# Kernel tuning notes

Hardware: AMD Instinct MI355X
Metric: run time of the kernel (lower is better)

Reference implementation:

```python
import jax, jax.numpy as jnp
import numpy as np

N_BRANCH, N_LAYER = 4, 3
B, T, D_IN = 4, 1024, 32
D_MODEL, D_INNER, D_STATE, D_CONV, DT_RANK = 128, 256, 16, 4, 8
EMBED = 64
MAX_NORM = 10.0  # safe_expmap0 tangent-norm clip
EPS = 1e-7


def setup_inputs() -> dict:
    key = jax.random.key(0)
    ks = jax.random.split(key, 12)
    def nrm(k, shp, s=0.02):
        return s * jax.random.normal(k, shp, dtype=jnp.float32)
    A_init = jnp.log(jnp.arange(1, D_STATE + 1, dtype=jnp.float32))
    return {
        "trend": jax.random.normal(ks[0], (B, T, D_IN), jnp.float32),
        "seasonal_coarse": jax.random.normal(ks[1], (B, T, D_IN), jnp.float32),
        "seasonal_fine": jax.random.normal(ks[2], (B, T, D_IN), jnp.float32),
        "residual": jax.random.normal(ks[3], (B, T, D_IN), jnp.float32),
        "W_ip": nrm(ks[4], (N_BRANCH, D_IN, D_MODEL)),
        "b_ip": jnp.zeros((N_BRANCH, D_MODEL), jnp.float32),
        "W_in": nrm(ks[5], (N_BRANCH, N_LAYER, D_MODEL, 2 * D_INNER)),
        "conv_w": nrm(ks[6], (N_BRANCH, N_LAYER, D_INNER, D_CONV), 0.1),
        "conv_b": jnp.zeros((N_BRANCH, N_LAYER, D_INNER), jnp.float32),
        "W_x": nrm(ks[7], (N_BRANCH, N_LAYER, D_INNER, DT_RANK + 2 * D_STATE)),
        "W_dt": nrm(ks[8], (N_BRANCH, N_LAYER, DT_RANK, D_INNER), 0.1),
        "b_dt": jnp.full((N_BRANCH, N_LAYER, D_INNER), -4.6, jnp.float32),  # softplus ~ 0.01
        "A_log": jnp.broadcast_to(A_init, (N_BRANCH, N_LAYER, D_INNER, D_STATE)),
        "D_param": jnp.ones((N_BRANCH, N_LAYER, D_INNER), jnp.float32),
        "W_out": nrm(ks[9], (N_BRANCH, N_LAYER, D_INNER, D_MODEL)),
        "W_op": nrm(ks[10], (N_BRANCH, D_MODEL, EMBED)),
        "b_op": jnp.zeros((N_BRANCH, EMBED), jnp.float32),
        "eff_scale": jnp.asarray(0.1, jnp.float32),
    }


def _mamba_layer(x, Win, cw, cb, Wx, Wdt, bdt, Alog, Dp, Wout):
    # x: [B, T, d_model]
    Tlen = x.shape[1]
    xz = x @ Win                                   # [B,T,2*di]
    xp, z = jnp.split(xz, 2, axis=-1)
    # causal depthwise conv1d, kernel D_CONV
    xpad = jnp.pad(xp, ((0, 0), (D_CONV - 1, 0), (0, 0)))
    xc = sum(xpad[:, k:k + Tlen, :] * cw[:, k] for k in range(D_CONV))
    xc = jax.nn.silu(xc + cb)                      # [B,T,di]
    dbl = xc @ Wx                                  # [B,T,r+2s]
    dt = jax.nn.softplus(dbl[..., :DT_RANK] @ Wdt + bdt)   # [B,T,di]
    Bm = dbl[..., DT_RANK:DT_RANK + D_STATE]       # [B,T,s]
    Cm = dbl[..., DT_RANK + D_STATE:]              # [B,T,s]
    A = -jnp.exp(Alog)                             # [di,s]
    dA = jnp.exp(dt[..., None] * A)                # [B,T,di,s]
    dBx = (dt * xc)[..., None] * Bm[:, :, None, :] # [B,T,di,s]

    def step(h, inp):
        dA_t, dBx_t, C_t = inp
        h = dA_t * h + dBx_t
        return h, jnp.einsum('bds,bs->bd', h, C_t)

    h0 = jnp.zeros((x.shape[0], D_INNER, D_STATE), x.dtype)
    _, ys = jax.lax.scan(step, h0, (jnp.swapaxes(dA, 0, 1),
                                     jnp.swapaxes(dBx, 0, 1),
                                     jnp.swapaxes(Cm, 0, 1)))
    y = jnp.swapaxes(ys, 0, 1) + Dp * xc
    return (y * jax.nn.silu(z)) @ Wout


def _embed(x, Wip, bip, Wins, cws, cbs, Wxs, Wdts, bdts, Alogs, Dps, Wouts, Wop, bop):
    h = x @ Wip + bip
    for l in range(N_LAYER):
        h = _mamba_layer(h, Wins[l], cws[l], cbs[l], Wxs[l], Wdts[l], bdts[l],
                         Alogs[l], Dps[l], Wouts[l])
    return h.mean(axis=1) @ Wop + bop              # [B, EMBED]


def _expmap0(v):
    # safe expmap0 on Lorentz (k=1): clip tangent norm at MAX_NORM
    n = jnp.linalg.norm(v, axis=-1, keepdims=True)
    nc = jnp.clip(n, EPS, MAX_NORM)
    v = v * (nc / jnp.maximum(n, EPS))
    return jnp.concatenate([jnp.cosh(nc), jnp.sinh(nc) / nc * v], axis=-1)


def _projx(x):
    sp = x[..., 1:]
    t = jnp.sqrt(1.0 + jnp.sum(sp * sp, axis=-1, keepdims=True))
    return jnp.concatenate([t, sp], axis=-1)


def _logmap0(x):
    sp = x[..., 1:]
    t = jnp.maximum(x[..., :1], 1.0 + EPS)
    d = jnp.arccosh(t)
    spn = jnp.maximum(jnp.linalg.norm(sp, axis=-1, keepdims=True), EPS)
    return d * sp / spn


def _forward(trend, seasonal_coarse, seasonal_fine, residual,
             W_ip, b_ip, W_in, conv_w, conv_b, W_x, W_dt, b_dt,
             A_log, D_param, W_out, W_op, b_op, eff_scale):
    xs = [trend, seasonal_coarse, seasonal_fine, residual]
    z_t = [
        _embed(xs[b], W_ip[b], b_ip[b], W_in[b], conv_w[b], conv_b[b], W_x[b],
               W_dt[b], b_dt[b], A_log[b], D_param[b], W_out[b], W_op[b], b_op[b])
        for b in range(N_BRANCH)
    ]
    es = jnp.tanh(eff_scale)
    z_h = [_projx(_expmap0(z * es)) for z in z_t]
    us = [_logmap0(zh) for zh in z_h]
    combined_tangent = us[0] + us[1] + us[2] + us[3]
    combined_h = _projx(_expmap0(combined_tangent * es))
    return (*z_t, *z_h, combined_tangent, combined_h)


def reference(trend, seasonal_coarse, seasonal_fine, residual,
              W_ip, b_ip, W_in, conv_w, conv_b, W_x, W_dt, b_dt,
              A_log, D_param, W_out, W_op, b_op, eff_scale):
    return _forward(trend, seasonal_coarse, seasonal_fine, residual,
                    W_ip, b_ip, W_in, conv_w, conv_b, W_x, W_dt, b_dt,
                    A_log, D_param, W_out, W_op, b_op, eff_scale)
```

## Files before the change

kernel.cpp:

```cpp
#include <hip/hip_runtime.h>
#include <math.h>

#define NBR 4
#define NLAY 3
#define Bk 4
#define Tk 1024
#define DIN 32
#define DMODEL 128
#define DINNER 256
#define DSTATE 16
#define DTRANK 8
#define EMBEDk 64
#define BT (Bk*Tk)
#define EPSF 1e-7f
#define MAXNF 10.0f
#define LCH 64
#define NCH (Tk/LCH)
#define UF 8
#define NWB 320

typedef __bf16 bf16x8 __attribute__((ext_vector_type(8)));
typedef float  f32x4  __attribute__((ext_vector_type(4)));
typedef unsigned short u16x8 __attribute__((ext_vector_type(8)));

__device__ __forceinline__ float siluf(float x){ return x / (1.f + __expf(-x)); }
__device__ __forceinline__ float softplusf(float x){ return (x > 20.f) ? x : log1pf(__expf(x)); }
__device__ __forceinline__ unsigned short f2b(float x){
    union { float f; unsigned u; } v; v.f = x;
    unsigned r = v.u + 0x7FFF + ((v.u >> 16) & 1);
    return (unsigned short)(r >> 16);
}
__device__ __forceinline__ float b2f(unsigned short u){
    union { unsigned u; float f; } v; v.u = ((unsigned)u) << 16; return v.f;
}

__device__ __forceinline__ void dA_pow(float q, float* dA){
    dA[0] = q;             dA[1] = q * q;
    dA[2] = dA[1] * dA[0]; dA[3] = dA[1] * dA[1];
    dA[4] = dA[3] * dA[0]; dA[5] = dA[3] * dA[1];
    dA[6] = dA[3] * dA[2]; dA[7] = dA[3] * dA[3];
    #pragma unroll
    for (int s = 8; s < 16; ++s) dA[s] = dA[s - 8] * dA[7];
}
__device__ __forceinline__ void dA_exp(float dtv, const float* Aa, float* dA){
    #pragma unroll
    for (int s = 0; s < 16; ++s) dA[s] = __expf(dtv * Aa[s]);
}

template<int MODE>
__global__ __launch_bounds__(256) void bgemm_k(
    const unsigned short* __restrict__ Ab, long aBr, int K,
    const unsigned short* __restrict__ Bt, long bBr,
    float* __restrict__ C0, long c0Br,
    float* __restrict__ C1, long c1Br,
    unsigned short* __restrict__ Cb, long cbBr,
    const float* __restrict__ bias, long biasBr)
{
    const int br = blockIdx.z;
    Ab += (long)br * aBr;
    Bt += (long)br * bBr;
    if (MODE == 1 || MODE == 3) C0 += (long)br * c0Br;
    if (MODE == 0 || MODE == 3) C1 += (long)br * c1Br;
    if (MODE == 0) Cb += (long)br * cbBr;
    if (MODE == 3) bias += (long)br * biasBr;
    const int m0 = blockIdx.x * 64, n0 = blockIdx.y * 64;
    __shared__ __align__(16) unsigned short As[8 * 64 * 8];
    __shared__ __align__(16) unsigned short Bs[8 * 64 * 8];
    const int tid = threadIdx.x;
    const int lane = tid & 63, w = tid >> 6;
    const int wm = w >> 1, wn = w & 1;
    const int quad = lane >> 4, l15 = lane & 15;
    f32x4 acc00 = {0,0,0,0}, acc01 = {0,0,0,0}, acc10 = {0,0,0,0}, acc11 = {0,0,0,0};
    for (int kc = 0; kc < K; kc += 64) {
        #pragma unroll
        for (int it = 0; it < 2; ++it) {
            const int c = tid + it * 256;
            const int r = c & 63, kch = c >> 6;
            *(u16x8*)&As[(kch * 64 + r) * 8] =
                *(const u16x8*)(Ab + (long)(m0 + r) * K + kc + kch * 8);
            *(u16x8*)&Bs[(kch * 64 + r) * 8] =
                *(const u16x8*)(Bt + (long)(n0 + r) * K + kc + kch * 8);
        }
        __syncthreads();
        #pragma unroll
        for (int k0 = 0; k0 < 64; k0 += 32) {
            const int kch = (k0 >> 3) + quad;
            bf16x8 a0 = *(const bf16x8*)&As[(kch * 64 + wm * 32 +      l15) * 8];
            bf16x8 a1 = *(const bf16x8*)&As[(kch * 64 + wm * 32 + 16 + l15) * 8];
            bf16x8 b0 = *(const bf16x8*)&Bs[(kch * 64 + wn * 32 +      l15) * 8];
            bf16x8 b1 = *(const bf16x8*)&Bs[(kch * 64 + wn * 32 + 16 + l15) * 8];
            acc00 = __builtin_amdgcn_mfma_f32_16x16x32_bf16(a0, b0, acc00, 0, 0, 0);
            acc01 = __builtin_amdgcn_mfma_f32_16x16x32_bf16(a0, b1, acc01, 0, 0, 0);
            acc10 = __builtin_amdgcn_mfma_f32_16x16x32_bf16(a1, b0, acc10, 0, 0, 0);
            acc11 = __builtin_amdgcn_mfma_f32_16x16x32_bf16(a1, b1, acc11, 0, 0, 0);
        }
        __syncthreads();
    }
    #pragma unroll
    for (int e = 0; e < 4; ++e) {
        f32x4 a = (e == 0) ? acc00 : (e == 1) ? acc01 : (e == 2) ? acc10 : acc11;
        const int msub = (e >> 1) * 16, nsub = (e & 1) * 16;
        const int col = n0 + wn * 32 + nsub + l15;
        #pragma unroll
        for (int r = 0; r < 4; ++r) {
            const int row = m0 + wm * 32 + msub + quad * 4 + r;
            const float v = a[r];
            if (MODE == 0) {
                if (n0 < 256) Cb[(long)row * 256 + col] = f2b(v);
                else          C1[(long)row * 256 + (col - 256)] = siluf(v);
            } else if (MODE == 1) {
                C0[(long)row * 128 + col] = v;
            } else {
                if (col < 256)      C0[(long)row * 256 + col] = softplusf(v + bias[col]);
                else if (col < 288) C1[(long)row * 32 + (col - 256)] = v;
            }
        }
    }
}

__global__ __launch_bounds__(256) void prepT_k(
    const float* __restrict__ W, unsigned short* __restrict__ o,
    int Kd, int Nd, long wBr, long oBr)
{
    const int br = blockIdx.z;
    W += (long)br * wBr; o += (long)br * oBr;
    const int n0 = blockIdx.x * 64, k0 = blockIdx.y * 64;
    __shared__ float tile[64][65];
    const int t = threadIdx.x;
    #pragma unroll
    for (int i = 0; i < 16; ++i) {
        int idx = t + i * 256;
        int kl = idx >> 6, nl = idx & 63;
        tile[kl][nl] = W[(long)(k0 + kl) * Nd + n0 + nl];
    }
    __syncthreads();
    #pragma unroll
    for (int i = 0; i < 16; ++i) {
        int idx = t + i * 256;
        int nl = idx >> 6, kl = idx & 63;
        o[(long)(n0 + nl) * Kd + k0 + kl] = f2b(tile[kl][nl]);
    }
}

__global__ __launch_bounds__(256) void sgemmW_k(
    const float* __restrict__ Wout, const float* __restrict__ Win,
    float* __restrict__ Wtmp)
{
    const int z = blockIdx.z, p = z >> 2, br = z & 3;
    const float* A  = Wout + (long)(br * NLAY + p) * DINNER * DMODEL;
    const float* Bw = Win  + (long)(br * NLAY + p + 1) * DMODEL * 512;
    float* C = Wtmp + (long)z * DINNER * 512;
    const int m0 = blockIdx.x * 64, n0 = blockIdx.y * 64;
    __shared__ float As[32][68];
    __shared__ float Bs[32][68];
    const int tid = threadIdx.x;
    const int tx = tid & 15, ty = tid >> 4;
    float acc[4][4] = {};
    for (int kc = 0; kc < DMODEL; kc += 32) {
        #pragma unroll
        for (int it = 0; it < 2; ++it) {
            int id = tid + it * 256;
            int r = id >> 3, c4 = (id & 7) << 2;
            float4 v = *(const float4*)(A + (long)(m0 + r) * DMODEL + kc + c4);
            As[c4+0][r] = v.x; As[c4+1][r] = v.y; As[c4+2][r] = v.z; As[c4+3][r] = v.w;
            int rb = id >> 4, cb = (id & 15) << 2;
            *(float4*)&Bs[rb][cb] = *(const float4*)(Bw + (long)(kc + rb) * 512 + n0 + cb);
        }
        __syncthreads();
        #pragma unroll
        for (int kk = 0; kk < 32; ++kk) {
            float4 a4 = *(const float4*)&As[kk][ty << 2];
            float4 b4 = *(const float4*)&Bs[kk][tx << 2];
            float av[4] = {a4.x, a4.y, a4.z, a4.w};
            float bv[4] = {b4.x, b4.y, b4.z, b4.w};
            #pragma unroll
            for (int i = 0; i < 4; ++i)
                #pragma unroll
                for (int j = 0; j < 4; ++j)
                    acc[i][j] = fmaf(av[i], bv[j], acc[i][j]);
        }
        __syncthreads();
    }
    #pragma unroll
    for (int i = 0; i < 4; ++i) {
        int row = m0 + (ty << 2) + i, col = n0 + (tx << 2);
        float4 v4; v4.x = acc[i][0]; v4.y = acc[i][1]; v4.z = acc[i][2]; v4.w = acc[i][3];
        *(float4*)(C + (long)row * 512 + col) = v4;
    }
}

__global__ __launch_bounds__(256) void prepC_k(
    const float* __restrict__ Wx, const float* __restrict__ Wdt,
    unsigned short* __restrict__ o)
{
    const int n = blockIdx.x, bl = blockIdx.y;
    const int k = threadIdx.x;
    const float* WxP = Wx + (long)bl * DINNER * 40;
    float v;
    if (n < 256) {
        const float* WdtP = Wdt + (long)bl * DTRANK * DINNER;
        float s = 0.f;
        #pragma unroll
        for (int r = 0; r < 8; ++r) s = fmaf(WxP[k * 40 + r], WdtP[r * DINNER + n], s);
        v = s;
    } else if (n < 288) {
        v = WxP[k * 40 + 8 + (n - 256)];
    } else {
        v = 0.f;
    }
    o[(long)bl * NWB * DINNER + (long)n * DINNER + k] = f2b(v);
}

__global__ __launch_bounds__(256) void proj_k(
    const float* __restrict__ A0, const float* __restrict__ A1,
    const float* __restrict__ A2, const float* __restrict__ A3,
    const float* __restrict__ Bw, const float* __restrict__ bias,
    unsigned short* __restrict__ Cb)
{
    const int br = blockIdx.z;
    const float* A = (br == 1) ? A1 : (br == 2) ? A2 : (br == 3) ? A3 : A0;
    Bw   += (long)br * DIN * DMODEL;
    bias += (long)br * DMODEL;
    Cb   += (long)br * BT * DMODEL;
    const int m0 = blockIdx.x * 64, n0 = blockIdx.y * 64;
    __shared__ float As[32][68];
    __shared__ float Bs[32][68];
    const int tid = threadIdx.x;
    const int tx = tid & 15, ty = tid >> 4;
    float acc[4][4] = {};
    {
        #pragma unroll
        for (int it = 0; it < 2; ++it) {
            int id = tid + it * 256;
            int r = id >> 3, c4 = (id & 7) << 2;
            float4 v = *(const float4*)(A + (long)(m0 + r) * DIN + c4);
            As[c4+0][r] = v.x; As[c4+1][r] = v.y; As[c4+2][r] = v.z; As[c4+3][r] = v.w;
            int rb = id >> 4, cb = (id & 15) << 2;
            *(float4*)&Bs[rb][cb] = *(const float4*)(Bw + (long)rb * DMODEL + n0 + cb);
        }
        __syncthreads();
        #pragma unroll
        for (int kk = 0; kk < 32; ++kk) {
            float4 a4 = *(const float4*)&As[kk][ty << 2];
            float4 b4 = *(const float4*)&Bs[kk][tx << 2];
            float av[4] = {a4.x, a4.y, a4.z, a4.w};
            float bv[4] = {b4.x, b4.y, b4.z, b4.w};
            #pragma unroll
            for (int i = 0; i < 4; ++i)
                #pragma unroll
                for (int j = 0; j < 4; ++j)
                    acc[i][j] = fmaf(av[i], bv[j], acc[i][j]);
        }
    }
    const int col = n0 + (tx << 2);
    float bs[4];
    #pragma unroll
    for (int j = 0; j < 4; ++j) bs[j] = bias[col + j];
    #pragma unroll
    for (int i = 0; i < 4; ++i) {
        const int row = m0 + (ty << 2) + i;
        #pragma unroll
        for (int j = 0; j < 4; ++j)
            Cb[(long)row * DMODEL + col + j] = f2b(acc[i][j] + bs[j]);
    }
}

__global__ __launch_bounds__(256) void conv_k(
    const unsigned short* __restrict__ xp, const float* __restrict__ cw,
    const float* __restrict__ cb, unsigned short* __restrict__ xcb, int layer)
{
    const int br = blockIdx.y;
    const long base = (long)br * BT * DINNER;
    const int idx = blockIdx.x * 256 + threadIdx.x;
    const int d = idx & (DINNER - 1);
    const int row = idx >> 8;
    const int t = row & (Tk - 1);
    const float4 w4 = *(const float4*)(cw + ((long)(br * NLAY + layer) * DINNER + d) * 4);
    const float wv[4] = {w4.x, w4.y, w4.z, w4.w};
    float acc = cb[(br * NLAY + layer) * DINNER + d];
    const unsigned short* xpb = xp + base + idx;
    #pragma unroll
    for (int k = 0; k < 4; ++k) {
        int tt = t + k - 3;
        if (tt >= 0) acc = fmaf(b2f(xpb[(long)(k - 3) * DINNER]), wv[k], acc);
    }
    xcb[base + idx] = f2b(siluf(acc));
}

__global__ __launch_bounds__(256) void scan1_k(
    const float* __restrict__ dtb, const unsigned short* __restrict__ xcb,
    const float* __restrict__ bcb, const float* __restrict__ Alog,
    float* __restrict__ recbuf, int layer)
{
    const int c = blockIdx.x, b = blockIdx.y, br = blockIdx.z;
    const int d = threadIdx.x;
    const float* Ap = Alog + ((long)(br * NLAY + layer) * DINNER + d) * DSTATE;
    float Aa[16];
    bool pw = true;
    #pragma unroll
    for (int s = 0; s < 16; ++s) {
        Aa[s] = -__expf(Ap[s]);
        pw = pw && (fabsf(Aa[s] + (float)(s + 1)) < 1e-3f);
    }
    const long rbase = (long)br * BT + (long)b * Tk + (long)c * LCH;
    const float* dtp = dtb + rbase * DINNER + d;
    const unsigned short* xcp = xcb + rbase * DINNER + d;
    __shared__ float bcs[LCH * 32];
    {
        const float4* g = (const float4*)(bcb + rbase * 32);
        float4* l = (float4*)bcs;
        l[d] = g[d]; l[d + 256] = g[d + 256];
    }
    float dtc[UF], xcc[UF];
    #pragma unroll
    for (int u = 0; u < UF; ++u) {
        dtc[u] = dtp[(long)u * DINNER];
        xcc[u] = b2f(xcp[(long)u * DINNER]);
    }
    __syncthreads();
    float h[16];
    #pragma unroll
    for (int s = 0; s < 16; ++s) h[s] = 0.f;
    float sumdt = 0.f;
    for (int base = 0; base < LCH; base += UF) {
        const int nb = (base + UF < LCH) ? base + UF : base;
        float dtn[UF], xcn[UF];
        #pragma unroll
        for (int u = 0; u < UF; ++u) {
            dtn[u] = dtp[(long)(nb + u) * DINNER];
            xcn[u] = b2f(xcp[(long)(nb + u) * DINNER]);
        }
        #pragma unroll
        for (int u = 0; u < UF; ++u) {
            const int t = base + u;
            const float dtv = dtc[u];
            const float dtxc = dtv * xcc[u];
            sumdt += dtv;
            float dA[16];
            if (pw) dA_pow(__expf(-dtv), dA);
            else    dA_exp(dtv, Aa, dA);
            const float* bcT = bcs + t * 32;
            #pragma unroll
            for (int s = 0; s < 16; ++s)
                h[s] = fmaf(dA[s], h[s], dtxc * bcT[s]);
        }
        #pragma unroll
        for (int u = 0; u < UF; ++u) { dtc[u] = dtn[u]; xcc[u] = xcn[u]; }
    }
    float* sb = recbuf + (((long)(br * 4 + b) * (NCH - 1) + c) * 17) * 256 + d;
    #pragma unroll
    for (int s = 0; s < 16; ++s) sb[s * 256] = h[s];
    sb[16 * 256] = sumdt;
}

__global__ __launch_bounds__(256) void scan3_k(
    const float* __restrict__ dtb, const unsigned short* __restrict__ xcb,
    const float* __restrict__ bcb, const float* __restrict__ zb,
    const float* __restrict__ Alog, const float* __restrict__ Dpar,
    const float* __restrict__ recbuf, unsigned short* __restrict__ yzb, int layer)
{
    const int c = blockIdx.x, b = blockIdx.y, br = blockIdx.z;
    const int d = threadIdx.x;
    const float* Ap = Alog + ((long)(br * NLAY + layer) * DINNER + d) * DSTATE;
    float Aa[16];
    bool pw = true;
    #pragma unroll
    for (int s = 0; s < 16; ++s) {
        Aa[s] = -__expf(Ap[s]);
        pw = pw && (fabsf(Aa[s] + (float)(s + 1)) < 1e-3f);
    }
    float h[16];
    #pragma unroll
    for (int s = 0; s < 16; ++s) h[s] = 0.f;
    if (c > 0) {
        const float* recB = recbuf + ((long)(br * 4 + b) * (NCH - 1)) * 17 * 256 + d;
        float rh[16], rs;
        #pragma unroll
        for (int s = 0; s < 16; ++s) rh[s] = recB[s * 256];
        rs = recB[16 * 256];
        for (int cc = 0; cc < c; ++cc) {
            float nh[16], ns = 0.f;
            if (cc + 1 < c) {
                const float* r2 = recB + (long)(cc + 1) * 17 * 256;
                #pragma unroll
                for (int s = 0; s < 16; ++s) nh[s] = r2[s * 256];
                ns = r2[16 * 256];
            } else {
                #pragma unroll
                for (int s = 0; s < 16; ++s) nh[s] = 0.f;
            }
            float P[16];
            if (pw) dA_pow(__expf(-rs), P);
            else    dA_exp(rs, Aa, P);
            #pragma unroll
            for (int s = 0; s < 16; ++s) h[s] = fmaf(h[s], P[s], rh[s]);
            #pragma unroll
            for (int s = 0; s < 16; ++s) rh[s] = nh[s];
            rs = ns;
        }
    }
    const float Dp = Dpar[(br * NLAY + layer) * DINNER + d];
    const long rbase = (long)br * BT + (long)b * Tk + (long)c * LCH;
    const float* dtp = dtb + rbase * DINNER + d;
    const unsigned short* xcp = xcb + rbase * DINNER + d;
    const float* zp  = zb  + rbase * DINNER + d;
    unsigned short* yp = yzb + rbase * DINNER + d;
    __shared__ float bcs[LCH * 32];
    {
        const float4* g = (const float4*)(bcb + rbase * 32);
        float4* l = (float4*)bcs;
        l[d] = g[d]; l[d + 256] = g[d + 256];
    }
    float dtc[UF], xcc[UF], zc[UF];
    #pragma unroll
    for (int u = 0; u < UF; ++u) {
        dtc[u] = dtp[(long)u * DINNER];
        xcc[u] = b2f(xcp[(long)u * DINNER]);
        zc[u]  = zp[(long)u * DINNER];
    }
    __syncthreads();
    for (int base = 0; base < LCH; base += UF) {
        const int nb = (base + UF < LCH) ? base + UF : base;
        float dtn[UF], xcn[UF], zn[UF];
        #pragma unroll
        for (int u = 0; u < UF; ++u) {
            dtn[u] = dtp[(long)(nb + u) * DINNER];
            xcn[u] = b2f(xcp[(long)(nb + u) * DINNER]);
            zn[u]  = zp[(long)(nb + u) * DINNER];
        }
        #pragma unroll
        for (int u = 0; u < UF; ++u) {
            const int t = base + u;
            const float dtv = dtc[u], xcv = xcc[u];
            const float dtxc = dtv * xcv;
            float dA[16];
            if (pw) dA_pow(__expf(-dtv), dA);
            else    dA_exp(dtv, Aa, dA);
            const float* bcT = bcs + t * 32;
            #pragma unroll
            for (int s = 0; s < 16; ++s)
                h[s] = fmaf(dA[s], h[s], dtxc * bcT[s]);
            float y0 = 0.f, y1 = 0.f, y2 = 0.f, y3 = 0.f;
            #pragma unroll
            for (int s = 0; s < 16; s += 4) {
                y0 = fmaf(h[s+0], bcT[16+s+0], y0);
                y1 = fmaf(h[s+1], bcT[16+s+1], y1);
                y2 = fmaf(h[s+2], bcT[16+s+2], y2);
                y3 = fmaf(h[s+3], bcT[16+s+3], y3);
            }
            const float y = (y0 + y1) + (y2 + y3) + Dp * xcv;
            yp[(long)t * DINNER] = f2b(y * zc[u]);
        }
        #pragma unroll
        for (int u = 0; u < UF; ++u) { dtc[u] = dtn[u]; xcc[u] = xcn[u]; zc[u] = zn[u]; }
    }
}

__global__ __launch_bounds__(128) void meanop_k(
    const float* __restrict__ hbuf, const float* __restrict__ Wop,
    const float* __restrict__ bop, float* __restrict__ outzt)
{
    const int br = blockIdx.x >> 2, b = blockIdx.x & 3;
    const int tid = threadIdx.x;
    const float* hp = hbuf + ((long)br * BT + (long)b * Tk) * DMODEL + tid;
    float s = 0.f;
    for (int t = 0; t < Tk; ++t) s += hp[(long)t * DMODEL];
    __shared__ float hm[DMODEL];
    hm[tid] = s * (1.0f / Tk);
    __syncthreads();
    if (tid < EMBEDk) {
        float acc = bop[br * EMBEDk + tid];
        for (int k = 0; k < DMODEL; ++k)
            acc = fmaf(hm[k], Wop[(long)br * DMODEL * EMBEDk + k * EMBEDk + tid], acc);
        outzt[br * (Bk * EMBEDk) + b * EMBEDk + tid] = acc;
    }
}

__global__ __launch_bounds__(64) void final_k(
    const float* __restrict__ zt, float* __restrict__ out, const float* __restrict__ eff)
{
    const float es = tanhf(eff[0]);
    __shared__ float us[NBR][Bk][EMBEDk];
    const int t = threadIdx.x;
    if (t < 16) {
        const int br = t >> 2, b = t & 3;
        const float* z = zt + br * (Bk * EMBEDk) + b * EMBEDk;
        float n2 = 0.f;
        for (int e = 0; e < EMBEDk; ++e) { float v = z[e] * es; n2 = fmaf(v, v, n2); }
        const float n  = sqrtf(n2);
        const float nc = fminf(fmaxf(n, EPSF), MAXNF);
        const float sc = nc / fmaxf(n, EPSF);
        const float sh = sinhf(nc) / nc;
        const float fac = es * sc * sh;
        float* zh = out + 1024 + br * (Bk * (EMBEDk + 1)) + b * (EMBEDk + 1);
        float sp2 = 0.f;
        for (int e = 0; e < EMBEDk; ++e) {
            float spv = z[e] * fac;
            sp2 = fmaf(spv, spv, sp2);
            zh[1 + e] = spv;
            us[br][b][e] = spv;
        }
        const float t0 = sqrtf(1.f + sp2);
        zh[0] = t0;
        const float dd  = acoshf(fmaxf(t0, 1.f + EPSF));
        const float spn = fmaxf(sqrtf(sp2), EPSF);
        const float rr  = dd / spn;
        for (int e = 0; e < EMBEDk; ++e) us[br][b][e] *= rr;
    }
    __syncthreads();
    if (t < 4) {
        const int b = t;
        float ct[EMBEDk];
        float* cto = out + 2064 + b * EMBEDk;
        for (int e = 0; e < EMBEDk; ++e) {
            float v = us[0][b][e] + us[1][b][e] + us[2][b][e] + us[3][b][e];
            ct[e] = v; cto[e] = v;
        }
        float n2 = 0.f;
        for (int e = 0; e < EMBEDk; ++e) { float v = ct[e] * es; n2 = fmaf(v, v, n2); }
        const float n  = sqrtf(n2);
        const float nc = fminf(fmaxf(n, EPSF), MAXNF);
        const float sc = nc / fmaxf(n, EPSF);
        const float sh = sinhf(nc) / nc;
        const float fac = es * sc * sh;
        float* ch = out + 2320 + b * (EMBEDk + 1);
        float sp2 = 0.f;
        for (int e = 0; e < EMBEDk; ++e) {
            float spv = ct[e] * fac;
            sp2 = fmaf(spv, spv, sp2);
            ch[1 + e] = spv;
        }
        ch[0] = sqrtf(1.f + sp2);
    }
}

extern "C" void kernel_launch(void* const* d_in, const int* in_sizes, int n_in,
                              void* d_out, int out_size, void* d_ws, size_t ws_size,
                              hipStream_t stream)
{
    const float* X0 = (const float*)d_in[0];
    const float* X1 = (const float*)d_in[1];
    const float* X2 = (const float*)d_in[2];
    const float* X3 = (const float*)d_in[3];
    const float* W_ip   = (const float*)d_in[4];
    const float* b_ip   = (const float*)d_in[5];
    const float* W_in   = (const float*)d_in[6];
    const float* conv_w = (const float*)d_in[7];
    const float* conv_b = (const float*)d_in[8];
    const float* W_x    = (const float*)d_in[9];
    const float* W_dt   = (const float*)d_in[10];
    const float* b_dt   = (const float*)d_in[11];
    const float* A_log  = (const float*)d_in[12];
    const float* D_par  = (const float*)d_in[13];
    const float* W_out  = (const float*)d_in[14];
    const float* W_op   = (const float*)d_in[15];
    const float* b_op   = (const float*)d_in[16];
    const float* eff    = (const float*)d_in[17];
    float* out = (float*)d_out;
    float* ws  = (float*)d_ws;

    float* buf_z  = ws;
    float* buf_dt = buf_z  + (long)NBR * BT * DINNER;
    float* buf_bc = buf_dt + (long)NBR * BT * DINNER;
    float* buf_h  = buf_bc + (long)NBR * BT * 32;
    float* recbuf = buf_h  + (long)NBR * BT * DMODEL;
    float* Wtmp   = recbuf + (long)16 * (NCH - 1) * 17 * 256;
    unsigned short* h_bf  = (unsigned short*)(Wtmp + (long)8 * DINNER * 512);
    unsigned short* xp_bf = h_bf  + (long)NBR * BT * DMODEL;
    unsigned short* xc_bf = xp_bf + (long)NBR * BT * DINNER;
    unsigned short* yz_bf = xc_bf + (long)NBR * BT * DINNER;
    unsigned short* Win0T = yz_bf + (long)NBR * BT * DINNER;
    unsigned short* WfT   = Win0T + (long)NBR * 512 * DMODEL;
    unsigned short* WcT   = WfT   + (long)8 * 512 * DINNER;
    unsigned short* Wo2T  = WcT   + (long)NBR * NLAY * NWB * DINNER;

    prepT_k<<<dim3(8, 2, NBR), 256, 0, stream>>>(
        W_in, Win0T, DMODEL, 512, (long)NLAY * DMODEL * 512, (long)512 * DMODEL);
    sgemmW_k<<<dim3(4, 8, 8), 256, 0, stream>>>(W_out, W_in, Wtmp);
    prepT_k<<<dim3(8, 4, 8), 256, 0, stream>>>(
        Wtmp, WfT, DINNER, 512, (long)DINNER * 512, (long)512 * DINNER);
    prepC_k<<<dim3(NWB, NBR * NLAY), 256, 0, stream>>>(W_x, W_dt, WcT);
    prepT_k<<<dim3(2, 4, NBR), 256, 0, stream>>>(
        W_out + (long)2 * DINNER * DMODEL, Wo2T, DINNER, DMODEL,
        (long)NLAY * DINNER * DMODEL, (long)DMODEL * DINNER);

    proj_k<<<dim3(BT / 64, DMODEL / 64, NBR), 256, 0, stream>>>(
        X0, X1, X2, X3, W_ip, b_ip, h_bf);

    for (int l = 0; l < NLAY; ++l) {
        if (l == 0) {
            bgemm_k<0><<<dim3(BT / 64, 8, NBR), 256, 0, stream>>>(
                h_bf, (long)BT * DMODEL, DMODEL,
                Win0T, (long)512 * DMODEL,
                nullptr, 0, buf_z, (long)BT * DINNER,
                xp_bf, (long)BT * DINNER, nullptr, 0);
        } else {
            bgemm_k<0><<<dim3(BT / 64, 8, NBR), 256, 0, stream>>>(
                yz_bf, (long)BT * DINNER, DINNER,
                WfT + (long)(l - 1) * 4 * 512 * DINNER, (long)512 * DINNER,
                nullptr, 0, buf_z, (long)BT * DINNER,
                xp_bf, (long)BT * DINNER, nullptr, 0);
        }
        conv_k<<<dim3((BT * DINNER) / 256, NBR), 256, 0, stream>>>(
            xp_bf, conv_w, conv_b, xc_bf, l);
        bgemm_k<3><<<dim3(BT / 64, NWB / 64, NBR), 256, 0, stream>>>(
            xc_bf, (long)BT * DINNER, DINNER,
            WcT + (long)l * NWB * DINNER, (long)NLAY * NWB * DINNER,
            buf_dt, (long)BT * DINNER, buf_bc, (long)BT * 32,
            nullptr, 0, b_dt + l * DINNER, (long)NLAY * DINNER);
        scan1_k<<<dim3(NCH - 1, Bk, NBR), 256, 0, stream>>>(
            buf_dt, xc_bf, buf_bc, A_log, recbuf, l);
        scan3_k<<<dim3(NCH, Bk, NBR), 256, 0, stream>>>(
            buf_dt, xc_bf, buf_bc, buf_z, A_log, D_par, recbuf, yz_bf, l);
        if (l == NLAY - 1) {
            bgemm_k<1><<<dim3(BT / 64, DMODEL / 64, NBR), 256, 0, stream>>>(
                yz_bf, (long)BT * DINNER, DINNER,
                Wo2T, (long)DMODEL * DINNER,
                buf_h, (long)BT * DMODEL, nullptr, 0,
                nullptr, 0, nullptr, 0);
        }
    }

    meanop_k<<<16, 128, 0, stream>>>(buf_h, W_op, b_op, out);
    final_k<<<1, 64, 0, stream>>>(out, out, eff);
}
```

Baseline: 471.8 us.

## Fuse prep kernels, store z as bf16, and reduce the final GEMM into a mean via atomics

Merges the weight transpose, combined-weight prep and input projection kernels into one launch. The z gate is now stored as bf16 instead of fp32, halving its write and read traffic. The last output GEMM no longer writes the full hidden tensor; it reduces its tile into per-batch column sums with atomicAdd, and the output projection moves into final_k, removing meanop_k. This cuts launches and memory traffic, but float atomics make the summation order nondeterministic, the zero-init of the accumulator sits inside the sgemmW kernel, and bf16 z adds rounding error.

```diff
diff --git a/kernel.cpp b/kernel.cpp
--- a/kernel.cpp
+++ b/kernel.cpp
@@ -54,15 +54,17 @@
     float* __restrict__ C0, long c0Br,
     float* __restrict__ C1, long c1Br,
     unsigned short* __restrict__ Cb, long cbBr,
+    unsigned short* __restrict__ Cb2, long cb2Br,
+    float* __restrict__ Mb,
     const float* __restrict__ bias, long biasBr)
 {
     const int br = blockIdx.z;
     Ab += (long)br * aBr;
     Bt += (long)br * bBr;
-    if (MODE == 1 || MODE == 3) C0 += (long)br * c0Br;
-    if (MODE == 0 || MODE == 3) C1 += (long)br * c1Br;
-    if (MODE == 0) Cb += (long)br * cbBr;
-    if (MODE == 3) bias += (long)br * biasBr;
+    if (MODE == 3) { C0 += (long)br * c0Br; C1 += (long)br * c1Br;
+                     bias += (long)br * biasBr; }
+    if (MODE == 0) { Cb += (long)br * cbBr; Cb2 += (long)br * cb2Br; }
+    if (MODE == 1) { Mb += (long)br * (Bk * DMODEL); }
     const int m0 = blockIdx.x * 64, n0 = blockIdx.y * 64;
     __shared__ __align__(16) unsigned short As[8 * 64 * 8];
     __shared__ __align__(16) unsigned short Bs[8 * 64 * 8];
@@ -96,6 +98,16 @@
         }
         __syncthreads();
     }
+    if (MODE == 1) {
+        float s0 = 0.f, s1 = 0.f;
+        #pragma unroll
+        for (int r = 0; r < 4; ++r) { s0 += acc00[r] + acc10[r];
+                                      s1 += acc01[r] + acc11[r]; }
+        const int bidx = m0 >> 10;
+        atomicAdd(&Mb[bidx * DMODEL + n0 + wn * 32 + l15], s0);
+        atomicAdd(&Mb[bidx * DMODEL + n0 + wn * 32 + 16 + l15], s1);
+        return;
+    }
     #pragma unroll
     for (int e = 0; e < 4; ++e) {
         f32x4 a = (e == 0) ? acc00 : (e == 1) ? acc01 : (e == 2) ? acc10 : acc11;
@@ -107,9 +119,7 @@
             const float v = a[r];
             if (MODE == 0) {
                 if (n0 < 256) Cb[(long)row * 256 + col] = f2b(v);
-                else          C1[(long)row * 256 + (col - 256)] = siluf(v);
-            } else if (MODE == 1) {
-                C0[(long)row * 128 + col] = v;
+                else          Cb2[(long)row * 256 + (col - 256)] = f2b(siluf(v));
             } else {
                 if (col < 256)      C0[(long)row * 256 + col] = softplusf(v + bias[col]);
                 else if (col < 288) C1[(long)row * 32 + (col - 256)] = v;
@@ -118,34 +128,13 @@
     }
 }
 
-__global__ __launch_bounds__(256) void prepT_k(
-    const float* __restrict__ W, unsigned short* __restrict__ o,
-    int Kd, int Nd, long wBr, long oBr)
-{
-    const int br = blockIdx.z;
-    W += (long)br * wBr; o += (long)br * oBr;
-    const int n0 = blockIdx.x * 64, k0 = blockIdx.y * 64;
-    __shared__ float tile[64][65];
-    const int t = threadIdx.x;
-    #pragma unroll
-    for (int i = 0; i < 16; ++i) {
-        int idx = t + i * 256;
-        int kl = idx >> 6, nl = idx & 63;
-        tile[kl][nl] = W[(long)(k0 + kl) * Nd + n0 + nl];
-    }
-    __syncthreads();
-    #pragma unroll
-    for (int i = 0; i < 16; ++i) {
-        int idx = t + i * 256;
-        int nl = idx >> 6, kl = idx & 63;
-        o[(long)(n0 + nl) * Kd + k0 + kl] = f2b(tile[kl][nl]);
-    }
-}
-
 __global__ __launch_bounds__(256) void sgemmW_k(
     const float* __restrict__ Wout, const float* __restrict__ Win,
-    float* __restrict__ Wtmp)
-{
+    float* __restrict__ Wtmp, unsigned* __restrict__ zbuf)
+{
+    if (blockIdx.x == 0 && blockIdx.y == 0 && blockIdx.z == 0) {
+        for (int i = threadIdx.x; i < 4096; i += 256) zbuf[i] = 0u;
+    }
     const int z = blockIdx.z, p = z >> 2, br = z & 3;
     const float* A  = Wout + (long)(br * NLAY + p) * DINNER * DMODEL;
     const float* Bw = Win  + (long)(br * NLAY + p + 1) * DMODEL * 512;
@@ -189,53 +178,99 @@
     }
 }
 
-__global__ __launch_bounds__(256) void prepC_k(
-    const float* __restrict__ Wx, const float* __restrict__ Wdt,
-    unsigned short* __restrict__ o)
-{
-    const int n = blockIdx.x, bl = blockIdx.y;
-    const int k = threadIdx.x;
-    const float* WxP = Wx + (long)bl * DINNER * 40;
-    float v;
-    if (n < 256) {
-        const float* WdtP = Wdt + (long)bl * DTRANK * DINNER;
-        float s = 0.f;
-        #pragma unroll
-        for (int r = 0; r < 8; ++r) s = fmaf(WxP[k * 40 + r], WdtP[r * DINNER + n], s);
-        v = s;
-    } else if (n < 288) {
-        v = WxP[k * 40 + 8 + (n - 256)];
+__device__ void transposeTile(const float* __restrict__ W,
+                              unsigned short* __restrict__ o,
+                              int Kd, int Nd, int n0, int k0, float* smem)
+{
+    float (*tile)[65] = (float(*)[65])smem;
+    const int t = threadIdx.x;
+    #pragma unroll
+    for (int i = 0; i < 16; ++i) {
+        int idx = t + i * 256;
+        int kl = idx >> 6, nl = idx & 63;
+        tile[kl][nl] = W[(long)(k0 + kl) * Nd + n0 + nl];
+    }
+    __syncthreads();
+    #pragma unroll
+    for (int i = 0; i < 16; ++i) {
+        int idx = t + i * 256;
+        int nl = idx >> 6, kl = idx & 63;
+        o[(long)(n0 + nl) * Kd + k0 + kl] = f2b(tile[kl][nl]);
+    }
+}
+
+__global__ __launch_bounds__(256) void prepAll_k(
+    const float* __restrict__ W_in, const float* __restrict__ Wtmp,
+    const float* __restrict__ W_out,
+    const float* __restrict__ W_x, const float* __restrict__ W_dt,
+    const float* __restrict__ X0, const float* __restrict__ X1,
+    const float* __restrict__ X2, const float* __restrict__ X3,
+    const float* __restrict__ W_ip, const float* __restrict__ b_ip,
+    unsigned short* __restrict__ Win0T, unsigned short* __restrict__ WfT,
+    unsigned short* __restrict__ Wo2T, unsigned short* __restrict__ WcT,
+    unsigned short* __restrict__ h_bf)
+{
+    __shared__ float smem[32 * 68 * 2];
+    const int id = blockIdx.x;
+    if (id < 64) {
+        int br = id >> 4, rem = id & 15;
+        int nt = rem & 7, kt = rem >> 3;
+        transposeTile(W_in + (long)br * NLAY * DMODEL * 512,
+                      Win0T + (long)br * 512 * DMODEL,
+                      DMODEL, 512, nt * 64, kt * 64, smem);
+    } else if (id < 320) {
+        int id2 = id - 64;
+        int z = id2 >> 5, rem = id2 & 31;
+        int nt = rem & 7, kt = rem >> 3;
+        transposeTile(Wtmp + (long)z * DINNER * 512,
+                      WfT + (long)z * 512 * DINNER,
+                      DINNER, 512, nt * 64, kt * 64, smem);
+    } else if (id < 352) {
+        int id3 = id - 320;
+        int br = id3 >> 3, rem = id3 & 7;
+        int nt = rem & 1, kt = rem >> 1;
+        transposeTile(W_out + ((long)br * NLAY + 2) * DINNER * DMODEL,
+                      Wo2T + (long)br * DMODEL * DINNER,
+                      DINNER, DMODEL, nt * 64, kt * 64, smem);
+    } else if (id < 4192) {
+        int id4 = id - 352;
+        int bl = id4 / NWB, n = id4 % NWB;
+        const int k = threadIdx.x;
+        const float* WxP = W_x + (long)bl * DINNER * 40;
+        float v;
+        if (n < 256) {
+            const float* WdtP = W_dt + (long)bl * DTRANK * DINNER;
+            float s = 0.f;
+            #pragma unroll
+            for (int r = 0; r < 8; ++r)
+                s = fmaf(WxP[k * 40 + r], WdtP[r * DINNER + n], s);
+            v = s;
+        } else if (n < 288) {
+            v = WxP[k * 40 + 8 + (n - 256)];
+        } else {
+            v = 0.f;
+        }
+        WcT[(long)bl * NWB * DINNER + (long)n * DINNER + k] = f2b(v);
     } else {
-        v = 0.f;
-    }
-    o[(long)bl * NWB * DINNER + (long)n * DINNER + k] = f2b(v);
-}
-
-__global__ __launch_bounds__(256) void proj_k(
-    const float* __restrict__ A0, const float* __restrict__ A1,
-    const float* __restrict__ A2, const float* __restrict__ A3,
-    const float* __restrict__ Bw, const float* __restrict__ bias,
-    unsigned short* __restrict__ Cb)
-{
-    const int br = blockIdx.z;
-    const float* A = (br == 1) ? A1 : (br == 2) ? A2 : (br == 3) ? A3 : A0;
-    Bw   += (long)br * DIN * DMODEL;
-    bias += (long)br * DMODEL;
-    Cb   += (long)br * BT * DMODEL;
-    const int m0 = blockIdx.x * 64, n0 = blockIdx.y * 64;
-    __shared__ float As[32][68];
-    __shared__ float Bs[32][68];
-    const int tid = threadIdx.x;
-    const int tx = tid & 15, ty = tid >> 4;
-    float acc[4][4] = {};
-    {
+        int id5 = id - 4192;
+        int br = id5 >> 7, rem = id5 & 127;
+        int m0 = (rem & 63) * 64, n0 = (rem >> 6) * 64;
+        const float* A = (br == 1) ? X1 : (br == 2) ? X2 : (br == 3) ? X3 : X0;
+        const float* Bw = W_ip + (long)br * DIN * DMODEL;
+        const float* bias = b_ip + (long)br * DMODEL;
+        unsigned short* Cb = h_bf + (long)br * BT * DMODEL;
+        float (*As)[68] = (float(*)[68])smem;
+        float (*Bs)[68] = (float(*)[68])(smem + 32 * 68);
+        const int tid = threadIdx.x;
+        const int tx = tid & 15, ty = tid >> 4;
+        float acc[4][4] = {};
         #pragma unroll
         for (int it = 0; it < 2; ++it) {
-            int id = tid + it * 256;
-            int r = id >> 3, c4 = (id & 7) << 2;
+            int idd = tid + it * 256;
+            int r = idd >> 3, c4 = (idd & 7) << 2;
             float4 v = *(const float4*)(A + (long)(m0 + r) * DIN + c4);
             As[c4+0][r] = v.x; As[c4+1][r] = v.y; As[c4+2][r] = v.z; As[c4+3][r] = v.w;
-            int rb = id >> 4, cb = (id & 15) << 2;
+            int rb = idd >> 4, cb = (idd & 15) << 2;
             *(float4*)&Bs[rb][cb] = *(const float4*)(Bw + (long)rb * DMODEL + n0 + cb);
         }
         __syncthreads();
@@ -251,17 +286,14 @@
                 for (int j = 0; j < 4; ++j)
                     acc[i][j] = fmaf(av[i], bv[j], acc[i][j]);
         }
-    }
-    const int col = n0 + (tx << 2);
-    float bs[4];
-    #pragma unroll
-    for (int j = 0; j < 4; ++j) bs[j] = bias[col + j];
-    #pragma unroll
-    for (int i = 0; i < 4; ++i) {
-        const int row = m0 + (ty << 2) + i;
-        #pragma unroll
-        for (int j = 0; j < 4; ++j)
-            Cb[(long)row * DMODEL + col + j] = f2b(acc[i][j] + bs[j]);
+        const int col = n0 + (tx << 2);
+        #pragma unroll
+        for (int i = 0; i < 4; ++i) {
+            const int row = m0 + (ty << 2) + i;
+            #pragma unroll
+            for (int j = 0; j < 4; ++j)
+                Cb[(long)row * DMODEL + col + j] = f2b(acc[i][j] + bias[col + j]);
+        }
     }
 }
 
@@ -355,7 +387,7 @@
 
 __global__ __launch_bounds__(256) void scan3_k(
     const float* __restrict__ dtb, const unsigned short* __restrict__ xcb,
-    const float* __restrict__ bcb, const float* __restrict__ zb,
+    const float* __restrict__ bcb, const unsigned short* __restrict__ zb,
     const float* __restrict__ Alog, const float* __restrict__ Dpar,
     const float* __restrict__ recbuf, unsigned short* __restrict__ yzb, int layer)
 {
@@ -403,7 +435,7 @@
     const long rbase = (long)br * BT + (long)b * Tk + (long)c * LCH;
     const float* dtp = dtb + rbase * DINNER + d;
     const unsigned short* xcp = xcb + rbase * DINNER + d;
-    const float* zp  = zb  + rbase * DINNER + d;
+    const unsigned short* zp  = zb  + rbase * DINNER + d;
     unsigned short* yp = yzb + rbase * DINNER + d;
     __shared__ float bcs[LCH * 32];
     {
@@ -416,7 +448,7 @@
     for (int u = 0; u < UF; ++u) {
         dtc[u] = dtp[(long)u * DINNER];
         xcc[u] = b2f(xcp[(long)u * DINNER]);
-        zc[u]  = zp[(long)u * DINNER];
+        zc[u]  = b2f(zp[(long)u * DINNER]);
     }
     __syncthreads();
     for (int base = 0; base < LCH; base += UF) {
@@ -426,7 +458,7 @@
         for (int u = 0; u < UF; ++u) {
             dtn[u] = dtp[(long)(nb + u) * DINNER];
             xcn[u] = b2f(xcp[(long)(nb + u) * DINNER]);
-            zn[u]  = zp[(long)(nb + u) * DINNER];
+            zn[u]  = b2f(zp[(long)(nb + u) * DINNER]);
         }
         #pragma unroll
         for (int u = 0; u < UF; ++u) {
@@ -456,35 +488,33 @@
     }
 }
 
-__global__ __launch_bounds__(128) void meanop_k(
-    const float* __restrict__ hbuf, const float* __restrict__ Wop,
-    const float* __restrict__ bop, float* __restrict__ outzt)
-{
-    const int br = blockIdx.x >> 2, b = blockIdx.x & 3;
-    const int tid = threadIdx.x;
-    const float* hp = hbuf + ((long)br * BT + (long)b * Tk) * DMODEL + tid;
-    float s = 0.f;
-    for (int t = 0; t < Tk; ++t) s += hp[(long)t * DMODEL];
-    __shared__ float hm[DMODEL];
-    hm[tid] = s * (1.0f / Tk);
-    __syncthreads();
-    if (tid < EMBEDk) {
-        float acc = bop[br * EMBEDk + tid];
-        for (int k = 0; k < DMODEL; ++k)
-            acc = fmaf(hm[k], Wop[(long)br * DMODEL * EMBEDk + k * EMBEDk + tid], acc);
-        outzt[br * (Bk * EMBEDk) + b * EMBEDk + tid] = acc;
-    }
-}
-
 __global__ __launch_bounds__(64) void final_k(
-    const float* __restrict__ zt, float* __restrict__ out, const float* __restrict__ eff)
-{
-    const float es = tanhf(eff[0]);
+    const float* __restrict__ Mb, const float* __restrict__ Wop,
+    const float* __restrict__ bop, float* __restrict__ out,
+    const float* __restrict__ eff)
+{
+    __shared__ float hm[NBR * Bk * DMODEL];
+    __shared__ float zts[NBR * Bk * EMBEDk];
     __shared__ float us[NBR][Bk][EMBEDk];
     const int t = threadIdx.x;
+    for (int i = t; i < NBR * Bk * DMODEL; i += 64) hm[i] = Mb[i] * (1.0f / Tk);
+    __syncthreads();
+    for (int br = 0; br < NBR; ++br) {
+        const float* wp = Wop + (long)br * DMODEL * EMBEDk + t;
+        const float bb = bop[br * EMBEDk + t];
+        for (int b = 0; b < Bk; ++b) {
+            const float* hmp = &hm[(br * Bk + b) * DMODEL];
+            float acc = bb;
+            for (int k = 0; k < DMODEL; ++k) acc = fmaf(hmp[k], wp[k * EMBEDk], acc);
+            out[(br * Bk + b) * EMBEDk + t] = acc;
+            zts[(br * Bk + b) * EMBEDk + t] = acc;
+        }
+    }
+    __syncthreads();
+    const float es = tanhf(eff[0]);
     if (t < 16) {
         const int br = t >> 2, b = t & 3;
-        const float* z = zt + br * (Bk * EMBEDk) + b * EMBEDk;
+        const float* z = &zts[(br * Bk + b) * EMBEDk];
         float n2 = 0.f;
         for (int e = 0; e < EMBEDk; ++e) { float v = z[e] * es; n2 = fmaf(v, v, n2); }
         const float n  = sqrtf(n2);
@@ -559,47 +589,40 @@
     float* out = (float*)d_out;
     float* ws  = (float*)d_ws;
 
-    float* buf_z  = ws;
-    float* buf_dt = buf_z  + (long)NBR * BT * DINNER;
+    float* meanb  = ws + 1024;
+    float* buf_dt = ws + 4096;
     float* buf_bc = buf_dt + (long)NBR * BT * DINNER;
-    float* buf_h  = buf_bc + (long)NBR * BT * 32;
-    float* recbuf = buf_h  + (long)NBR * BT * DMODEL;
+    float* recbuf = buf_bc + (long)NBR * BT * 32;
     float* Wtmp   = recbuf + (long)16 * (NCH - 1) * 17 * 256;
     unsigned short* h_bf  = (unsigned short*)(Wtmp + (long)8 * DINNER * 512);
     unsigned short* xp_bf = h_bf  + (long)NBR * BT * DMODEL;
-    unsigned short* xc_bf = xp_bf + (long)NBR * BT * DINNER;
+    unsigned short* z_bf  = xp_bf + (long)NBR * BT * DINNER;
+    unsigned short* xc_bf = z_bf  + (long)NBR * BT * DINNER;
     unsigned short* yz_bf = xc_bf + (long)NBR * BT * DINNER;
     unsigned short* Win0T = yz_bf + (long)NBR * BT * DINNER;
     unsigned short* WfT   = Win0T + (long)NBR * 512 * DMODEL;
-    unsigned short* WcT   = WfT   + (long)8 * 512 * DINNER;
-    unsigned short* Wo2T  = WcT   + (long)NBR * NLAY * NWB * DINNER;
-
-    prepT_k<<<dim3(8, 2, NBR), 256, 0, stream>>>(
-        W_in, Win0T, DMODEL, 512, (long)NLAY * DMODEL * 512, (long)512 * DMODEL);
-    sgemmW_k<<<dim3(4, 8, 8), 256, 0, stream>>>(W_out, W_in, Wtmp);
-    prepT_k<<<dim3(8, 4, 8), 256, 0, stream>>>(
-        Wtmp, WfT, DINNER, 512, (long)DINNER * 512, (long)512 * DINNER);
-    prepC_k<<<dim3(NWB, NBR * NLAY), 256, 0, stream>>>(W_x, W_dt, WcT);
-    prepT_k<<<dim3(2, 4, NBR), 256, 0, stream>>>(
-        W_out + (long)2 * DINNER * DMODEL, Wo2T, DINNER, DMODEL,
-        (long)NLAY * DINNER * DMODEL, (long)DMODEL * DINNER);
-
-    proj_k<<<dim3(BT / 64, DMODEL / 64, NBR), 256, 0, stream>>>(
-        X0, X1, X2, X3, W_ip, b_ip, h_bf);
+    unsigned short* Wo2T  = WfT   + (long)8 * 512 * DINNER;
+    unsigned short* WcT   = Wo2T  + (long)NBR * DMODEL * DINNER;
+
+    sgemmW_k<<<dim3(4, 8, 8), 256, 0, stream>>>(W_out, W_in, Wtmp, (unsigned*)ws);
+    prepAll_k<<<4704, 256, 0, stream>>>(
+        W_in, Wtmp, W_out, W_x, W_dt, X0, X1, X2, X3, W_ip, b_ip,
+        Win0T, WfT, Wo2T, WcT, h_bf);
 
     for (int l = 0; l < NLAY; ++l) {
         if (l == 0) {
             bgemm_k<0><<<dim3(BT / 64, 8, NBR), 256, 0, stream>>>(
-                h_bf, (long)BT * DMODEL, DMODEL,
-                Win0T, (long)512 * DMODEL,
-                nullptr, 0, buf_z, (long)BT * DINNER,
-                xp_bf, (long)BT * DINNER, nullptr, 0);
+                h_bf, (long)BT * DMODEL, DMODEL, Win0T, (long)512 * DMODEL,
+                nullptr, 0, nullptr, 0,
+                xp_bf, (long)BT * DINNER, z_bf, (long)BT * DINNER,
+                nullptr, nullptr, 0);
         } else {
             bgemm_k<0><<<dim3(BT / 64, 8, NBR), 256, 0, stream>>>(
                 yz_bf, (long)BT * DINNER, DINNER,
                 WfT + (long)(l - 1) * 4 * 512 * DINNER, (long)512 * DINNER,
-                nullptr, 0, buf_z, (long)BT * DINNER,
-                xp_bf, (long)BT * DINNER, nullptr, 0);
+                nullptr, 0, nullptr, 0,
+                xp_bf, (long)BT * DINNER, z_bf, (long)BT * DINNER,
+                nullptr, nullptr, 0);
         }
         conv_k<<<dim3((BT * DINNER) / 256, NBR), 256, 0, stream>>>(
             xp_bf, conv_w, conv_b, xc_bf, l);
@@ -607,20 +630,20 @@
             xc_bf, (long)BT * DINNER, DINNER,
             WcT + (long)l * NWB * DINNER, (long)NLAY * NWB * DINNER,
             buf_dt, (long)BT * DINNER, buf_bc, (long)BT * 32,
-            nullptr, 0, b_dt + l * DINNER, (long)NLAY * DINNER);
+            nullptr, 0, nullptr, 0,
+            nullptr, b_dt + l * DINNER, (long)NLAY * DINNER);
         scan1_k<<<dim3(NCH - 1, Bk, NBR), 256, 0, stream>>>(
             buf_dt, xc_bf, buf_bc, A_log, recbuf, l);
         scan3_k<<<dim3(NCH, Bk, NBR), 256, 0, stream>>>(
-            buf_dt, xc_bf, buf_bc, buf_z, A_log, D_par, recbuf, yz_bf, l);
+            buf_dt, xc_bf, buf_bc, z_bf, A_log, D_par, recbuf, yz_bf, l);
         if (l == NLAY - 1) {
             bgemm_k<1><<<dim3(BT / 64, DMODEL / 64, NBR), 256, 0, stream>>>(
                 yz_bf, (long)BT * DINNER, DINNER,
                 Wo2T, (long)DMODEL * DINNER,
-                buf_h, (long)BT * DMODEL, nullptr, 0,
-                nullptr, 0, nullptr, 0);
-        }
-    }
-
-    meanop_k<<<16, 128, 0, stream>>>(buf_h, W_op, b_op, out);
-    final_k<<<1, 64, 0, stream>>>(out, out, eff);
-}
+                nullptr, 0, nullptr, 0, nullptr, 0, nullptr, 0,
+                meanb, nullptr, 0);
+        }
+    }
+
+    final_k<<<1, 64, 0, stream>>>(meanb, W_op, b_op, out, eff);
+}
```

Result: no change. 477.3 us (+1.2%).
